# Kernel tuning notes

Hardware: AMD Instinct MI355X
Metric: run time of the kernel (lower is better)

## Reference

```python
import jax, jax.numpy as jnp
import numpy as np

N, E = 50000, 800000
IN_DIM, H, OUT_DIM = 128, 32, 128


def _p(key, shape, fan_in):
    return jax.random.normal(key, shape, dtype=jnp.float32) / np.float32(np.sqrt(fan_in))


def gcn(x, edge_index, W, b):
    # GCNConv with DOUBLED self-loops (outer add_self_loops + gcn_norm's own):
    # deg[i] = in_degree(i) + 2, each node receives 2*dinv[i]^2 * h[i].
    src, dst = edge_index[0], edge_index[1]
    h = x @ W  # [N, out]
    deg = jnp.zeros((x.shape[0],), h.dtype).at[dst].add(1.0) + 2.0
    dinv = jax.lax.rsqrt(deg)
    coef = dinv[src] * dinv[dst]  # [E]
    agg = jax.ops.segment_sum(h[src] * coef[:, None], dst, num_segments=x.shape[0])
    agg = agg + (2.0 * dinv * dinv)[:, None] * h
    return agg + b


def multihop(x, edge_index, W, b, fW, fb):
    # hop loop in the source always re-uses initial_x -> collapses to 1 pass
    return gcn(x, edge_index, W, b) @ fW + fb


def deconv(xc, W, b):
    # ConvTranspose1d(kernel=2, stride=2): out[n,o,2l+t] = sum_c xc[n,c,l]*W[c,o,t] + b[o]
    y = jnp.einsum('ncl,cot->nolt', xc, W) + b[None, :, None, None]
    return y.reshape(y.shape[0], y.shape[1], -1)  # [N, O, 2L]


def setup_inputs() -> dict:
    key = jax.random.key(0)
    ks = jax.random.split(key, 30)
    return {
        'x': jax.random.normal(ks[0], (N, IN_DIM), jnp.float32),
        'edge_index': jax.random.randint(ks[1], (2, E), 0, N),
        'w_enc1': _p(ks[2], (IN_DIM, H), IN_DIM), 'b_enc1': _p(ks[3], (H,), H),
        'fw_enc1': _p(ks[4], (H, H), H), 'fb_enc1': _p(ks[5], (H,), H),
        'w_enc2': _p(ks[6], (H, 2 * H), H), 'b_enc2': _p(ks[7], (2 * H,), 2 * H),
        'fw_enc2': _p(ks[8], (2 * H, 2 * H), 2 * H), 'fb_enc2': _p(ks[9], (2 * H,), 2 * H),
        'w_enc3': _p(ks[10], (2 * H, 4 * H), 2 * H), 'b_enc3': _p(ks[11], (4 * H,), 4 * H),
        'fw_enc3': _p(ks[12], (4 * H, 4 * H), 4 * H), 'fb_enc3': _p(ks[13], (4 * H,), 4 * H),
        'wd1': _p(ks[14], (4 * H, 2 * H, 2), 4 * H), 'bd1': _p(ks[15], (2 * H,), 4 * H),
        'wd2': _p(ks[16], (2 * H, H, 2), 2 * H), 'bd2': _p(ks[17], (H,), 2 * H),
        'wd3': _p(ks[18], (H, H, 2), H), 'bd3': _p(ks[19], (H,), H),
        'ws1': _p(ks[20], (2 * H, 2 * H), 2 * H), 'bs1': _p(ks[21], (2 * H,), 2 * H),
        'ws2': _p(ks[22], (H, H), H), 'bs2': _p(ks[23], (H,), H),
        'wf': _p(ks[24], (8 * H, OUT_DIM), 8 * H), 'bf': _p(ks[25], (OUT_DIM,), 8 * H),
    }


def reference(x, edge_index, w_enc1, b_enc1, fw_enc1, fb_enc1,
              w_enc2, b_enc2, fw_enc2, fb_enc2,
              w_enc3, b_enc3, fw_enc3, fb_enc3,
              wd1, bd1, wd2, bd2, wd3, bd3,
              ws1, bs1, ws2, bs2, wf, bf):
    relu = jax.nn.relu
    x1 = relu(multihop(x, edge_index, w_enc1, b_enc1, fw_enc1, fb_enc1))   # [N, H]
    x2 = relu(multihop(x1, edge_index, w_enc2, b_enc2, fw_enc2, fb_enc2))  # [N, 2H]
    x3 = relu(multihop(x2, edge_index, w_enc3, b_enc3, fw_enc3, fb_enc3))  # [N, 4H]
    d = deconv(x3[:, :, None], wd1, bd1)            # [N, 2H, 2]
    s2 = x2 @ ws1 + bs1                              # skip_conv1 (k=1) == linear
    d = d + s2[:, :, None]                           # repeat over length
    d = deconv(d, wd2, bd2)                          # [N, H, 4]
    s1 = x1 @ ws2 + bs2
    d = d + s1[:, :, None]
    d = deconv(d, wd3, bd3)                          # [N, H, 8]
    out = d.reshape(d.shape[0], -1) @ wf + bf        # [N, OUT_DIM]
    return out
```

## Files before the change

kernel.cpp:

```cpp
#include <hip/hip_runtime.h>

#define NN 50000
#define NE 800000
#define NBLK 196

typedef _Float16 half8 __attribute__((ext_vector_type(8)));
typedef _Float16 half4 __attribute__((ext_vector_type(4)));
typedef float f32x4v __attribute__((ext_vector_type(4)));

__global__ void k_zero2(int* __restrict__ bcnt) {
  bcnt[threadIdx.x] = 0;
}

__launch_bounds__(256)
__global__ void k_bcount(const int* __restrict__ dstv, int* __restrict__ bcnt) {
  __shared__ int cnt[256];
  int t = threadIdx.x;
  int e0 = blockIdx.x * 4096;
  cnt[t] = 0;
  __syncthreads();
#pragma unroll
  for (int i = 0; i < 16; ++i) {
    int e = e0 + i * 256 + t;
    if (e < NE) atomicAdd(&cnt[dstv[e] >> 8], 1);
  }
  __syncthreads();
  if (cnt[t] > 0) atomicAdd(&bcnt[t], cnt[t]);
}

__global__ void k_bscan(const int* __restrict__ bcnt, int* __restrict__ boff,
                        int* __restrict__ bcur, int* __restrict__ row_start) {
  __shared__ int s[256];
  int t = threadIdx.x;
  int v0 = (t < NBLK) ? bcnt[t] : 0;
  s[t] = v0;
  __syncthreads();
  for (int off = 1; off < 256; off <<= 1) {
    int v = (t >= off) ? s[t - off] : 0;
    __syncthreads();
    s[t] += v;
    __syncthreads();
  }
  int e = s[t] - v0;
  if (t < NBLK) { boff[t] = e; bcur[t] = e; }
  if (t == 0) { boff[NBLK] = NE; row_start[NN] = NE; }
}

__launch_bounds__(256)
__global__ void k_part1(const int* __restrict__ srcv, const int* __restrict__ dstv,
                        int* __restrict__ bcur, unsigned int* __restrict__ epk2) {
  __shared__ int cnt[256];
  __shared__ int base[256];
  int t = threadIdx.x;
  int e0 = blockIdx.x * 4096;
  cnt[t] = 0;
  __syncthreads();
  unsigned int pk[16];
  int lo[16], bk[16];
  bool ok[16];
#pragma unroll
  for (int i = 0; i < 16; ++i) {
    int e = e0 + i * 256 + t;
    ok[i] = (e < NE);
    if (ok[i]) {
      int s = srcv[e], d = dstv[e];
      bk[i] = d >> 8;
      pk[i] = (unsigned int)s | ((unsigned int)(d & 255) << 16);
      lo[i] = atomicAdd(&cnt[bk[i]], 1);
    }
  }
  __syncthreads();
  int c = cnt[t];
  if (c > 0) base[t] = atomicAdd(&bcur[t], c);
  __syncthreads();
#pragma unroll
  for (int i = 0; i < 16; ++i)
    if (ok[i]) epk2[base[bk[i]] + lo[i]] = pk[i];
}

__launch_bounds__(256)
__global__ void k_part2c(const unsigned int* __restrict__ epk2, const int* __restrict__ boff,
                         int* __restrict__ row_start, float* __restrict__ dinv,
                         float* __restrict__ rdinv, unsigned short* __restrict__ esrc) {
  __shared__ int cnt[256];
  __shared__ int cur[256];
  __shared__ int ss[256];
  int t = threadIdx.x;
  int b = blockIdx.x;
  int rs0 = boff[b], rs1 = boff[b + 1];
  cnt[t] = 0;
  __syncthreads();
  for (int i = rs0 + t; i < rs1; i += 256) {
    unsigned int p = epk2[i];
    atomicAdd(&cnt[(p >> 16) & 255], 1);
  }
  __syncthreads();
  int d = cnt[t];
  ss[t] = d;
  __syncthreads();
  for (int off = 1; off < 256; off <<= 1) {
    int v = (t >= off) ? ss[t - off] : 0;
    __syncthreads();
    ss[t] += v;
    __syncthreads();
  }
  int rs = rs0 + ss[t] - d;
  int node = b * 256 + t;
  if (node < NN) {
    row_start[node] = rs;
    float df = (float)d + 2.0f;
    dinv[node] = rsqrtf(df);
    rdinv[node] = sqrtf(df);
  }
  cur[t] = rs;
  __syncthreads();
  for (int i = rs0 + t; i < rs1; i += 256) {
    unsigned int p = epk2[i];
    int dl = (p >> 16) & 255;
    int tgt = atomicAdd(&cur[dl], 1);
    esrc[tgt] = (unsigned short)(p & 0xFFFFu);
  }
}

__global__ void k_prep1(const float* __restrict__ wd3, const float* __restrict__ wf,
                        const float* __restrict__ w2, const float* __restrict__ fw2,
                        const float* __restrict__ w3, const float* __restrict__ fw3,
                        const float* __restrict__ b1, const float* __restrict__ fw1,
                        const float* __restrict__ fb1,
                        const float* __restrict__ b2, const float* __restrict__ fb2,
                        const float* __restrict__ b3, const float* __restrict__ fb3,
                        float* __restrict__ G,
                        float* __restrict__ Wc2, float* __restrict__ Wc3,
                        float* __restrict__ bc1, float* __restrict__ bc2,
                        float* __restrict__ bc3) {
  int id = blockIdx.x * 256 + threadIdx.x;
  if (id < 16384) {
    int k = id & 127, r = id >> 7;
    int c = r >> 2, l = r & 3;
    float s = 0.f;
    for (int o = 0; o < 32; ++o) {
      s = fmaf(wd3[c * 64 + o * 2 + 0], wf[(o * 8 + 2 * l + 0) * 128 + k], s);
      s = fmaf(wd3[c * 64 + o * 2 + 1], wf[(o * 8 + 2 * l + 1) * 128 + k], s);
    }
    G[r * 128 + k] = s;
    return;
  }
  int id2 = id - 16384;
  if (id2 < 2048) {
    int c = id2 >> 6, k = id2 & 63;
    float s = 0.f;
    for (int j = 0; j < 64; ++j) s = fmaf(w2[c * 64 + j], fw2[j * 64 + k], s);
    Wc2[id2] = s;
  } else if (id2 < 10240) {
    int idx = id2 - 2048;
    int c = idx >> 7, k = idx & 127;
    float s = 0.f;
    for (int j = 0; j < 128; ++j) s = fmaf(w3[c * 128 + j], fw3[j * 128 + k], s);
    Wc3[idx] = s;
  } else if (id2 < 10272) {
    int k = id2 - 10240;
    float s = fb1[k];
    for (int j = 0; j < 32; ++j) s = fmaf(b1[j], fw1[j * 32 + k], s);
    bc1[k] = s;
  } else if (id2 < 10336) {
    int k = id2 - 10272;
    float s = fb2[k];
    for (int j = 0; j < 64; ++j) s = fmaf(b2[j], fw2[j * 64 + k], s);
    bc2[k] = s;
  } else if (id2 < 10464) {
    int k = id2 - 10336;
    float s = fb3[k];
    for (int j = 0; j < 128; ++j) s = fmaf(b3[j], fw3[j * 128 + k], s);
    bc3[k] = s;
  }
}

__global__ void k_prep_HA1(const float* __restrict__ wd2, const float* __restrict__ G,
                           const float* __restrict__ ws2,
                           float* __restrict__ Hm, float* __restrict__ A1) {
  int id = blockIdx.x * 256 + threadIdx.x;
  if (id < 16384) {
    int k = id & 127, r = id >> 7;
    int c = r >> 1, l = r & 1;
    float s = 0.f;
    for (int o = 0; o < 32; ++o) {
      s = fmaf(wd2[c * 64 + o * 2 + 0], G[(o * 4 + 2 * l + 0) * 128 + k], s);
      s = fmaf(wd2[c * 64 + o * 2 + 1], G[(o * 4 + 2 * l + 1) * 128 + k], s);
    }
    Hm[r * 128 + k] = s;
  } else if (id < 16384 + 4096) {
    int idx = id - 16384;
    int k = idx & 127, c = idx >> 7;
    float s = 0.f;
    for (int o = 0; o < 32; ++o) {
      float g = G[(4 * o) * 128 + k] + G[(4 * o + 1) * 128 + k] +
                G[(4 * o + 2) * 128 + k] + G[(4 * o + 3) * 128 + k];
      s = fmaf(ws2[c * 32 + o], g, s);
    }
    A1[c * 128 + k] = s;
  }
}

__global__ void k_prep_A32c0(const float* __restrict__ wd1, const float* __restrict__ ws1,
                             const float* __restrict__ Hm, const float* __restrict__ G,
                             const float* __restrict__ wf,
                             const float* __restrict__ bd1, const float* __restrict__ bs1,
                             const float* __restrict__ bd2, const float* __restrict__ bs2,
                             const float* __restrict__ bd3, const float* __restrict__ bf,
                             float* __restrict__ A3, float* __restrict__ A2,
                             float* __restrict__ c0) {
  int id = blockIdx.x * 256 + threadIdx.x;
  if (id < 16384) {
    int k = id & 127, c = id >> 7;
    float s = 0.f;
    for (int j = 0; j < 128; ++j) s = fmaf(wd1[c * 128 + j], Hm[j * 128 + k], s);
    A3[c * 128 + k] = s;
  } else if (id < 16384 + 8192) {
    int idx = id - 16384;
    int k = idx & 127, c = idx >> 7;
    float s = 0.f;
    for (int o = 0; o < 64; ++o)
      s = fmaf(ws1[c * 64 + o], Hm[(2 * o) * 128 + k] + Hm[(2 * o + 1) * 128 + k], s);
    A2[c * 128 + k] = s;
  } else if (id < 16384 + 8192 + 128) {
    int k = id - 16384 - 8192;
    float s = bf[k];
    for (int o = 0; o < 64; ++o) {
      float b = bd1[o] + bs1[o];
      s = fmaf(b, Hm[(o * 2) * 128 + k] + Hm[(o * 2 + 1) * 128 + k], s);
    }
    for (int o = 0; o < 32; ++o) {
      float b = bd2[o] + bs2[o];
      float g = G[(o * 4) * 128 + k] + G[(o * 4 + 1) * 128 + k] +
                G[(o * 4 + 2) * 128 + k] + G[(o * 4 + 3) * 128 + k];
      s = fmaf(b, g, s);
    }
    for (int o = 0; o < 32; ++o) {
      float w8 = 0.f;
      for (int j = 0; j < 8; ++j) w8 += wf[(o * 8 + j) * 128 + k];
      s = fmaf(bd3[o], w8, s);
    }
    c0[k] = s;
  }
}

__global__ void k_prep_pack(const float* __restrict__ Wc3, const float* __restrict__ Acat,
                            _Float16* __restrict__ W3pk, _Float16* __restrict__ Apk) {
  int id = blockIdx.x * 256 + threadIdx.x;
  if (id < 1024) {
    int l = id & 63, nb = (id >> 6) & 7, kb = id >> 9;
    int kbase = kb * 32 + ((l >> 4) << 3);
    int col = nb * 16 + (l & 15);
#pragma unroll
    for (int j = 0; j < 8; ++j)
      W3pk[id * 8 + j] = (_Float16)Wc3[(kbase + j) * 128 + col];
  } else if (id < 1024 + 3584) {
    int idx = id - 1024;
    int l = idx & 63, nb = (idx >> 6) & 7, kb = idx >> 9;
    int kbase = kb * 32 + ((l >> 4) << 3);
    int col = nb * 16 + (l & 15);
#pragma unroll
    for (int j = 0; j < 8; ++j)
      Apk[idx * 8 + j] = (_Float16)Acat[(kbase + j) * 128 + col];
  }
}

__launch_bounds__(256)
__global__ void k_gemm1t(const float* __restrict__ X, const float* __restrict__ W,
                         const float* __restrict__ dinv, _Float16* __restrict__ Yh) {
  __shared__ float sW[128 * 32];
  __shared__ float sXc[128 * 33];
  int t = threadIdx.x;
  int n0 = blockIdx.x * 128;
#pragma unroll
  for (int it = 0; it < 4; ++it) {
    int idx = t + it * 256;
    int kr = idx >> 3, c4 = (idx & 7) * 4;
    *reinterpret_cast<float4*>(&sW[kr * 32 + c4]) =
        *reinterpret_cast<const float4*>(&W[kr * 32 + c4]);
  }
  int rg = t >> 3;
  int cg = t & 7;
  float acc[4][4];
#pragma unroll
  for (int r = 0; r < 4; ++r)
#pragma unroll
    for (int c = 0; c < 4; ++c) acc[r][c] = 0.f;

  for (int ch = 0; ch < 4; ++ch) {
    __syncthreads();
#pragma unroll
    for (int it = 0; it < 4; ++it) {
      int idx = t + it * 256;
      int row = idx & 127, k4 = (idx >> 7) * 4;
      int n = n0 + row;
      float4 v = make_float4(0.f, 0.f, 0.f, 0.f);
      if (n < NN) v = *reinterpret_cast<const float4*>(&X[(size_t)n * 128 + ch * 32 + k4]);
      sXc[row * 33 + k4 + 0] = v.x;
      sXc[row * 33 + k4 + 1] = v.y;
      sXc[row * 33 + k4 + 2] = v.z;
      sXc[row * 33 + k4 + 3] = v.w;
    }
    __syncthreads();
#pragma unroll
    for (int k = 0; k < 32; ++k) {
      float4 w = *reinterpret_cast<const float4*>(&sW[(ch * 32 + k) * 32 + cg * 4]);
#pragma unroll
      for (int r = 0; r < 4; ++r) {
        float xv = sXc[(rg * 4 + r) * 33 + k];
        acc[r][0] = fmaf(xv, w.x, acc[r][0]);
        acc[r][1] = fmaf(xv, w.y, acc[r][1]);
        acc[r][2] = fmaf(xv, w.z, acc[r][2]);
        acc[r][3] = fmaf(xv, w.w, acc[r][3]);
      }
    }
  }
#pragma unroll
  for (int r = 0; r < 4; ++r) {
    int n = n0 + rg * 4 + r;
    if (n < NN) {
      float dv = dinv[n];
      half4 hv;
      hv[0] = (_Float16)(dv * acc[r][0]); hv[1] = (_Float16)(dv * acc[r][1]);
      hv[2] = (_Float16)(dv * acc[r][2]); hv[3] = (_Float16)(dv * acc[r][3]);
      *reinterpret_cast<half4*>(&Yh[(size_t)n * 32 + cg * 4]) = hv;
    }
  }
}

__device__ inline float4 gsum32h(const half4* __restrict__ H4,
                                 const unsigned short* __restrict__ esrc,
                                 const int* __restrict__ row_start,
                                 int n, int fg, int way) {
  float4 acc = make_float4(0.f, 0.f, 0.f, 0.f);
  if (way == 0) {
    half4 h = H4[(size_t)n * 8 + fg];
    acc.x = 2.f * (float)h[0]; acc.y = 2.f * (float)h[1];
    acc.z = 2.f * (float)h[2]; acc.w = 2.f * (float)h[3];
  }
  int end = row_start[n + 1];
  int i = row_start[n] + way;
  for (; i + 4 < end; i += 8) {
    int s0 = esrc[i], s1 = esrc[i + 4];
    half4 a = H4[(size_t)s0 * 8 + fg];
    half4 b = H4[(size_t)s1 * 8 + fg];
    acc.x += (float)a[0] + (float)b[0];
    acc.y += (float)a[1] + (float)b[1];
    acc.z += (float)a[2] + (float)b[2];
    acc.w += (float)a[3] + (float)b[3];
  }
  if (i < end) {
    int s = esrc[i];
    half4 a = H4[(size_t)s * 8 + fg];
    acc.x += (float)a[0]; acc.y += (float)a[1];
    acc.z += (float)a[2]; acc.w += (float)a[3];
  }
  acc.x += __shfl_xor(acc.x, 8);  acc.y += __shfl_xor(acc.y, 8);
  acc.z += __shfl_xor(acc.z, 8);  acc.w += __shfl_xor(acc.w, 8);
  acc.x += __shfl_xor(acc.x, 16); acc.y += __shfl_xor(acc.y, 16);
  acc.z += __shfl_xor(acc.z, 16); acc.w += __shfl_xor(acc.w, 16);
  return acc;
}

__launch_bounds__(256)
__global__ void k_fuse1(const _Float16* __restrict__ H, const unsigned short* __restrict__ esrc,
                        const int* __restrict__ row_start, const float* __restrict__ dinv,
                        const float* __restrict__ W, const float* __restrict__ bias,
                        _Float16* __restrict__ Y) {
  __shared__ float sZT[32][9];
  __shared__ float sW[32 * 32];
  int t = threadIdx.x;
  int n0 = blockIdx.x * 8;
  {
    int kr = t >> 3, c4 = (t & 7) * 4;
    *reinterpret_cast<float4*>(&sW[kr * 32 + c4]) =
        *reinterpret_cast<const float4*>(&W[kr * 32 + c4]);
  }
  int node = t >> 5, fg = t & 7, way = (t >> 3) & 3;
  int n = n0 + node;
  float4 z = gsum32h(reinterpret_cast<const half4*>(H), esrc, row_start, n, fg, way);
  if (way == 0) {
    float dv = dinv[n];
    sZT[fg * 4 + 0][node] = dv * z.x;
    sZT[fg * 4 + 1][node] = dv * z.y;
    sZT[fg * 4 + 2][node] = dv * z.z;
    sZT[fg * 4 + 3][node] = dv * z.w;
  }
  __syncthreads();
  int nd = t >> 5, col = t & 31;
  float a = bias[col];
#pragma unroll
  for (int k = 0; k < 32; ++k) a = fmaf(sZT[k][nd], sW[k * 32 + col], a);
  Y[(size_t)(n0 + nd) * 32 + col] = (_Float16)(dinv[n0 + nd] * fmaxf(a, 0.f));
}

__launch_bounds__(256)
__global__ void k_fuse2(const _Float16* __restrict__ H, const unsigned short* __restrict__ esrc,
                        const int* __restrict__ row_start, const float* __restrict__ dinv,
                        const float* __restrict__ W, const float* __restrict__ bias,
                        _Float16* __restrict__ Y) {
  __shared__ float sZT[32][9];
  __shared__ float sW[32 * 64];
  int t = threadIdx.x;
  int n0 = blockIdx.x * 8;
#pragma unroll
  for (int it = 0; it < 2; ++it) {
    int idx = t + it * 256;
    int kr = idx >> 4, c4 = (idx & 15) * 4;
    *reinterpret_cast<float4*>(&sW[kr * 64 + c4]) =
        *reinterpret_cast<const float4*>(&W[kr * 64 + c4]);
  }
  int node = t >> 5, fg = t & 7, way = (t >> 3) & 3;
  int n = n0 + node;
  float4 z = gsum32h(reinterpret_cast<const half4*>(H), esrc, row_start, n, fg, way);
  if (way == 0) {
    float dv = dinv[n];
    sZT[fg * 4 + 0][node] = dv * z.x;
    sZT[fg * 4 + 1][node] = dv * z.y;
    sZT[fg * 4 + 2][node] = dv * z.z;
    sZT[fg * 4 + 3][node] = dv * z.w;
  }
  __syncthreads();
  int nd = t >> 5, col = t & 31;
  float a = bias[col], b = bias[col + 32];
#pragma unroll
  for (int k = 0; k < 32; ++k) {
    float zv = sZT[k][nd];
    a = fmaf(zv, sW[k * 64 + col], a);
    b = fmaf(zv, sW[k * 64 + col + 32], b);
  }
  float dv = dinv[n0 + nd];
  Y[(size_t)(n0 + nd) * 64 + col] = (_Float16)(dv * fmaxf(a, 0.f));
  Y[(size_t)(n0 + nd) * 64 + col + 32] = (_Float16)(dv * fmaxf(b, 0.f));
}

__launch_bounds__(256)
__global__ void k_gath64(const _Float16* __restrict__ H, const unsigned short* __restrict__ esrc,
                         const int* __restrict__ row_start, const float* __restrict__ dinv,
                         _Float16* __restrict__ Zh) {
  int t = threadIdx.x;
  int n = blockIdx.x * 4 + (t >> 6);
  int fg = t & 15, way = (t >> 4) & 3;
  const half4* H4 = reinterpret_cast<const half4*>(H);
  float4 acc = make_float4(0.f, 0.f, 0.f, 0.f);
  if (way == 0) {
    half4 h = H4[(size_t)n * 16 + fg];
    acc.x = 2.f * (float)h[0]; acc.y = 2.f * (float)h[1];
    acc.z = 2.f * (float)h[2]; acc.w = 2.f * (float)h[3];
  }
  int end = row_start[n + 1];
  int i = row_start[n] + way;
  for (; i + 4 < end; i += 8) {
    int s0 = esrc[i], s1 = esrc[i + 4];
    half4 a = H4[(size_t)s0 * 16 + fg];
    half4 b = H4[(size_t)s1 * 16 + fg];
    acc.x += (float)a[0] + (float)b[0];
    acc.y += (float)a[1] + (float)b[1];
    acc.z += (float)a[2] + (float)b[2];
    acc.w += (float)a[3] + (float)b[3];
  }
  if (i < end) {
    int s = esrc[i];
    half4 a = H4[(size_t)s * 16 + fg];
    acc.x += (float)a[0]; acc.y += (float)a[1];
    acc.z += (float)a[2]; acc.w += (float)a[3];
  }
  acc.x += __shfl_xor(acc.x, 16); acc.y += __shfl_xor(acc.y, 16);
  acc.z += __shfl_xor(acc.z, 16); acc.w += __shfl_xor(acc.w, 16);
  acc.x += __shfl_xor(acc.x, 32); acc.y += __shfl_xor(acc.y, 32);
  acc.z += __shfl_xor(acc.z, 32); acc.w += __shfl_xor(acc.w, 32);
  if (way == 0) {
    float dv = dinv[n];
    half4 hv;
    hv[0] = (_Float16)(dv * acc.x); hv[1] = (_Float16)(dv * acc.y);
    hv[2] = (_Float16)(dv * acc.z); hv[3] = (_Float16)(dv * acc.w);
    *reinterpret_cast<half4*>(Zh + (size_t)n * 64 + fg * 4) = hv;
  }
}

__device__ inline half8 cvt8h(const _Float16* __restrict__ p, float s) {
  half8 v = *reinterpret_cast<const half8*>(p);
  half8 a;
#pragma unroll
  for (int i = 0; i < 8; ++i) a[i] = (_Float16)(s * (float)v[i]);
  return a;
}

__launch_bounds__(256)
__global__ void k_decode(const _Float16* __restrict__ z3h, const _Float16* __restrict__ X2h,
                         const _Float16* __restrict__ X1h, const float* __restrict__ rdinv,
                         const half8* __restrict__ W3pk, const half8* __restrict__ Apk,
                         const float* __restrict__ bc3, const float* __restrict__ c0,
                         float* __restrict__ out) {
  __shared__ _Float16 sX3[4][16][136];
  int t = threadIdx.x;
  int w = t >> 6, l = t & 63;
  int m16 = l & 15, g = l >> 4;
  int n0 = blockIdx.x * 64 + w * 16;
  int nrow = n0 + m16;

  f32x4v acc[8];
#pragma unroll
  for (int nb = 0; nb < 8; ++nb) {
    float bv = bc3[nb * 16 + m16];
    acc[nb] = (f32x4v){bv, bv, bv, bv};
  }
#pragma unroll
  for (int kb = 0; kb < 2; ++kb) {
    half8 a = *reinterpret_cast<const half8*>(z3h + (size_t)nrow * 64 + kb * 32 + g * 8);
#pragma unroll
    for (int nb = 0; nb < 8; ++nb) {
      half8 b = W3pk[(kb * 8 + nb) * 64 + l];
      acc[nb] = __builtin_amdgcn_mfma_f32_16x16x32_f16(a, b, acc[nb], 0, 0, 0);
    }
  }
#pragma unroll
  for (int nb = 0; nb < 8; ++nb)
#pragma unroll
    for (int r = 0; r < 4; ++r)
      sX3[w][g * 4 + r][nb * 16 + m16] = (_Float16)fmaxf(acc[nb][r], 0.0f);
  __syncthreads();

  float rd = rdinv[nrow];
#pragma unroll
  for (int nb = 0; nb < 8; ++nb) {
    float cv = c0[nb * 16 + m16];
    acc[nb] = (f32x4v){cv, cv, cv, cv};
  }
#pragma unroll
  for (int kb = 0; kb < 7; ++kb) {
    half8 a;
    if (kb < 4)
      a = *reinterpret_cast<const half8*>(&sX3[w][m16][kb * 32 + g * 8]);
    else if (kb < 6)
      a = cvt8h(X2h + (size_t)nrow * 64 + (kb - 4) * 32 + g * 8, rd);
    else
      a = cvt8h(X1h + (size_t)nrow * 32 + g * 8, rd);
#pragma unroll
    for (int nb = 0; nb < 8; ++nb) {
      half8 b = Apk[(kb * 8 + nb) * 64 + l];
      acc[nb] = __builtin_amdgcn_mfma_f32_16x16x32_f16(a, b, acc[nb], 0, 0, 0);
    }
  }
#pragma unroll
  for (int nb = 0; nb < 8; ++nb)
#pragma unroll
    for (int r = 0; r < 4; ++r) {
      int n = n0 + g * 4 + r;
      if (n < NN) out[(size_t)n * 128 + nb * 16 + m16] = acc[nb][r];
    }
}

extern "C" void kernel_launch(void* const* d_in, const int* in_sizes, int n_in,
                              void* d_out, int out_size, void* d_ws, size_t ws_size,
                              hipStream_t stream) {
  const float* x   = (const float*)d_in[0];
  const int* ei    = (const int*)d_in[1];
  const int* srcv  = ei;
  const int* dstv  = ei + NE;
  const float* w1  = (const float*)d_in[2];
  const float* b1  = (const float*)d_in[3];
  const float* fw1 = (const float*)d_in[4];
  const float* fb1 = (const float*)d_in[5];
  const float* w2  = (const float*)d_in[6];
  const float* b2  = (const float*)d_in[7];
  const float* fw2 = (const float*)d_in[8];
  const float* fb2 = (const float*)d_in[9];
  const float* w3  = (const float*)d_in[10];
  const float* b3  = (const float*)d_in[11];
  const float* fw3 = (const float*)d_in[12];
  const float* fb3 = (const float*)d_in[13];
  const float* wd1 = (const float*)d_in[14];
  const float* bd1 = (const float*)d_in[15];
  const float* wd2 = (const float*)d_in[16];
  const float* bd2 = (const float*)d_in[17];
  const float* wd3 = (const float*)d_in[18];
  const float* bd3 = (const float*)d_in[19];
  const float* ws1 = (const float*)d_in[20];
  const float* bs1 = (const float*)d_in[21];
  const float* ws2 = (const float*)d_in[22];
  const float* bs2 = (const float*)d_in[23];
  const float* wf  = (const float*)d_in[24];
  const float* bf  = (const float*)d_in[25];

  float* fp = (float*)d_ws;
  float* dinv = fp;
  float* rdinv= dinv + 50176;
  _Float16* h1h = (_Float16*)(rdinv + 50176);
  _Float16* x1h = h1h + 1601536;
  _Float16* x2h = x1h + 1601536;
  _Float16* z3h = x2h + 3203072;
  float* Wc2  = (float*)(z3h + 3203072);
  float* Wc3  = Wc2 + 2048;
  float* bc1  = Wc3 + 8192;
  float* bc2  = bc1 + 64;
  float* bc3  = bc2 + 64;
  float* G    = bc3 + 128;
  float* Hm   = G + 16384;
  float* A3   = Hm + 16384;
  float* A2   = A3 + 16384;
  float* A1   = A2 + 8192;
  float* c0   = A1 + 4096;
  _Float16* W3pk = (_Float16*)(c0 + 256);
  _Float16* Apk  = W3pk + 8192;
  unsigned int* epk2 = (unsigned int*)(Apk + 28672);
  unsigned short* esrc = (unsigned short*)(epk2 + 800000);
  int* ip     = (int*)(esrc + 800128);
  int* row_start = ip;
  int* bcnt   = row_start + 50176;
  int* boff   = bcnt + 256;
  int* bcur   = boff + 260;

  float* outp = (float*)d_out;

  k_zero2<<<1, 256, 0, stream>>>(bcnt);
  k_bcount<<<(NE + 4095) / 4096, 256, 0, stream>>>(dstv, bcnt);
  k_bscan<<<1, 256, 0, stream>>>(bcnt, boff, bcur, row_start);
  k_part1<<<(NE + 4095) / 4096, 256, 0, stream>>>(srcv, dstv, bcur, epk2);
  k_part2c<<<NBLK, 256, 0, stream>>>(epk2, boff, row_start, dinv, rdinv, esrc);

  k_prep1<<<105, 256, 0, stream>>>(wd3, wf, w2, fw2, w3, fw3, b1, fw1, fb1,
                                   b2, fb2, b3, fb3, G, Wc2, Wc3, bc1, bc2, bc3);
  k_prep_HA1<<<80, 256, 0, stream>>>(wd2, G, ws2, Hm, A1);
  k_prep_A32c0<<<97, 256, 0, stream>>>(wd1, ws1, Hm, G, wf, bd1, bs1, bd2, bs2, bd3, bf,
                                       A3, A2, c0);
  k_prep_pack<<<18, 256, 0, stream>>>(Wc3, A3 , W3pk, Apk);

  k_gemm1t<<<(NN + 127) / 128, 256, 0, stream>>>(x, w1, dinv, h1h);
  k_fuse1<<<NN / 8, 256, 0, stream>>>(h1h, esrc, row_start, dinv, fw1, bc1, x1h);
  k_fuse2<<<NN / 8, 256, 0, stream>>>(x1h, esrc, row_start, dinv, Wc2, bc2, x2h);
  k_gath64<<<NN / 4, 256, 0, stream>>>(x2h, esrc, row_start, dinv, z3h);
  k_decode<<<(NN + 63) / 64, 256, 0, stream>>>(z3h, x2h, x1h, rdinv, (const half8*)W3pk,
                                               (const half8*)Apk, bc3, c0, outp);
}
```

Before: 171.2 us.

## Merge preprocessing kernels into four launches and move first GEMM to MFMA

Combines the CSR-construction stages with the weight-folding prep kernels into four multi-role launches, with block-index ranges choosing each role. This removes the zeroing and separate count launches by writing per-block bucket counts that the scan block then sums. The first dense projection now packs w1 to fp16 and computes on 16x16x32 fp16 MFMA instead of the fp32 shared-memory FMA kernel. This cuts launch count and serialization, at the cost of fp16 rounding of x and w1 and a serial 196-way reduction in the scan block.

```diff
diff --git a/kernel.cpp b/kernel.cpp
--- a/kernel.cpp
+++ b/kernel.cpp
@@ -8,177 +8,119 @@
 typedef _Float16 half4 __attribute__((ext_vector_type(4)));
 typedef float f32x4v __attribute__((ext_vector_type(4)));
 
-__global__ void k_zero2(int* __restrict__ bcnt) {
-  bcnt[threadIdx.x] = 0;
-}
-
-__launch_bounds__(256)
-__global__ void k_bcount(const int* __restrict__ dstv, int* __restrict__ bcnt) {
+__launch_bounds__(256)
+__global__ void k_u1(const int* __restrict__ dstv, int* __restrict__ bcnt2,
+                     const float* __restrict__ wd3, const float* __restrict__ wf,
+                     const float* __restrict__ w2, const float* __restrict__ fw2,
+                     const float* __restrict__ w3, const float* __restrict__ fw3,
+                     const float* __restrict__ b1, const float* __restrict__ fw1,
+                     const float* __restrict__ fb1,
+                     const float* __restrict__ b2, const float* __restrict__ fb2,
+                     const float* __restrict__ b3, const float* __restrict__ fb3,
+                     float* __restrict__ G,
+                     float* __restrict__ Wc2, float* __restrict__ Wc3,
+                     float* __restrict__ bc1, float* __restrict__ bc2,
+                     float* __restrict__ bc3,
+                     const float* __restrict__ w1, _Float16* __restrict__ W1pk) {
   __shared__ int cnt[256];
   int t = threadIdx.x;
-  int e0 = blockIdx.x * 4096;
-  cnt[t] = 0;
-  __syncthreads();
-#pragma unroll
-  for (int i = 0; i < 16; ++i) {
-    int e = e0 + i * 256 + t;
-    if (e < NE) atomicAdd(&cnt[dstv[e] >> 8], 1);
-  }
-  __syncthreads();
-  if (cnt[t] > 0) atomicAdd(&bcnt[t], cnt[t]);
-}
-
-__global__ void k_bscan(const int* __restrict__ bcnt, int* __restrict__ boff,
-                        int* __restrict__ bcur, int* __restrict__ row_start) {
-  __shared__ int s[256];
-  int t = threadIdx.x;
-  int v0 = (t < NBLK) ? bcnt[t] : 0;
-  s[t] = v0;
-  __syncthreads();
-  for (int off = 1; off < 256; off <<= 1) {
-    int v = (t >= off) ? s[t - off] : 0;
-    __syncthreads();
-    s[t] += v;
-    __syncthreads();
-  }
-  int e = s[t] - v0;
-  if (t < NBLK) { boff[t] = e; bcur[t] = e; }
-  if (t == 0) { boff[NBLK] = NE; row_start[NN] = NE; }
-}
-
-__launch_bounds__(256)
-__global__ void k_part1(const int* __restrict__ srcv, const int* __restrict__ dstv,
-                        int* __restrict__ bcur, unsigned int* __restrict__ epk2) {
-  __shared__ int cnt[256];
-  __shared__ int base[256];
-  int t = threadIdx.x;
-  int e0 = blockIdx.x * 4096;
-  cnt[t] = 0;
-  __syncthreads();
-  unsigned int pk[16];
-  int lo[16], bk[16];
-  bool ok[16];
-#pragma unroll
-  for (int i = 0; i < 16; ++i) {
-    int e = e0 + i * 256 + t;
-    ok[i] = (e < NE);
-    if (ok[i]) {
-      int s = srcv[e], d = dstv[e];
-      bk[i] = d >> 8;
-      pk[i] = (unsigned int)s | ((unsigned int)(d & 255) << 16);
-      lo[i] = atomicAdd(&cnt[bk[i]], 1);
-    }
-  }
-  __syncthreads();
-  int c = cnt[t];
-  if (c > 0) base[t] = atomicAdd(&bcur[t], c);
-  __syncthreads();
-#pragma unroll
-  for (int i = 0; i < 16; ++i)
-    if (ok[i]) epk2[base[bk[i]] + lo[i]] = pk[i];
-}
-
-__launch_bounds__(256)
-__global__ void k_part2c(const unsigned int* __restrict__ epk2, const int* __restrict__ boff,
-                         int* __restrict__ row_start, float* __restrict__ dinv,
-                         float* __restrict__ rdinv, unsigned short* __restrict__ esrc) {
-  __shared__ int cnt[256];
-  __shared__ int cur[256];
-  __shared__ int ss[256];
-  int t = threadIdx.x;
   int b = blockIdx.x;
-  int rs0 = boff[b], rs1 = boff[b + 1];
-  cnt[t] = 0;
-  __syncthreads();
-  for (int i = rs0 + t; i < rs1; i += 256) {
-    unsigned int p = epk2[i];
-    atomicAdd(&cnt[(p >> 16) & 255], 1);
-  }
-  __syncthreads();
-  int d = cnt[t];
-  ss[t] = d;
-  __syncthreads();
-  for (int off = 1; off < 256; off <<= 1) {
-    int v = (t >= off) ? ss[t - off] : 0;
-    __syncthreads();
-    ss[t] += v;
-    __syncthreads();
-  }
-  int rs = rs0 + ss[t] - d;
-  int node = b * 256 + t;
-  if (node < NN) {
-    row_start[node] = rs;
-    float df = (float)d + 2.0f;
-    dinv[node] = rsqrtf(df);
-    rdinv[node] = sqrtf(df);
-  }
-  cur[t] = rs;
-  __syncthreads();
-  for (int i = rs0 + t; i < rs1; i += 256) {
-    unsigned int p = epk2[i];
-    int dl = (p >> 16) & 255;
-    int tgt = atomicAdd(&cur[dl], 1);
-    esrc[tgt] = (unsigned short)(p & 0xFFFFu);
-  }
-}
-
-__global__ void k_prep1(const float* __restrict__ wd3, const float* __restrict__ wf,
-                        const float* __restrict__ w2, const float* __restrict__ fw2,
-                        const float* __restrict__ w3, const float* __restrict__ fw3,
-                        const float* __restrict__ b1, const float* __restrict__ fw1,
-                        const float* __restrict__ fb1,
-                        const float* __restrict__ b2, const float* __restrict__ fb2,
-                        const float* __restrict__ b3, const float* __restrict__ fb3,
-                        float* __restrict__ G,
-                        float* __restrict__ Wc2, float* __restrict__ Wc3,
-                        float* __restrict__ bc1, float* __restrict__ bc2,
-                        float* __restrict__ bc3) {
-  int id = blockIdx.x * 256 + threadIdx.x;
-  if (id < 16384) {
-    int k = id & 127, r = id >> 7;
-    int c = r >> 2, l = r & 3;
-    float s = 0.f;
-    for (int o = 0; o < 32; ++o) {
-      s = fmaf(wd3[c * 64 + o * 2 + 0], wf[(o * 8 + 2 * l + 0) * 128 + k], s);
-      s = fmaf(wd3[c * 64 + o * 2 + 1], wf[(o * 8 + 2 * l + 1) * 128 + k], s);
-    }
-    G[r * 128 + k] = s;
+  if (b < NBLK) {
+    int e0 = b * 4096;
+    cnt[t] = 0;
+    __syncthreads();
+#pragma unroll
+    for (int i = 0; i < 16; ++i) {
+      int e = e0 + i * 256 + t;
+      if (e < NE) atomicAdd(&cnt[dstv[e] >> 8], 1);
+    }
+    __syncthreads();
+    bcnt2[b * 256 + t] = cnt[t];
     return;
   }
-  int id2 = id - 16384;
-  if (id2 < 2048) {
-    int c = id2 >> 6, k = id2 & 63;
-    float s = 0.f;
-    for (int j = 0; j < 64; ++j) s = fmaf(w2[c * 64 + j], fw2[j * 64 + k], s);
-    Wc2[id2] = s;
-  } else if (id2 < 10240) {
-    int idx = id2 - 2048;
-    int c = idx >> 7, k = idx & 127;
-    float s = 0.f;
-    for (int j = 0; j < 128; ++j) s = fmaf(w3[c * 128 + j], fw3[j * 128 + k], s);
-    Wc3[idx] = s;
-  } else if (id2 < 10272) {
-    int k = id2 - 10240;
-    float s = fb1[k];
-    for (int j = 0; j < 32; ++j) s = fmaf(b1[j], fw1[j * 32 + k], s);
-    bc1[k] = s;
-  } else if (id2 < 10336) {
-    int k = id2 - 10272;
-    float s = fb2[k];
-    for (int j = 0; j < 64; ++j) s = fmaf(b2[j], fw2[j * 64 + k], s);
-    bc2[k] = s;
-  } else if (id2 < 10464) {
-    int k = id2 - 10336;
-    float s = fb3[k];
-    for (int j = 0; j < 128; ++j) s = fmaf(b3[j], fw3[j * 128 + k], s);
-    bc3[k] = s;
-  }
-}
-
-__global__ void k_prep_HA1(const float* __restrict__ wd2, const float* __restrict__ G,
-                           const float* __restrict__ ws2,
-                           float* __restrict__ Hm, float* __restrict__ A1) {
-  int id = blockIdx.x * 256 + threadIdx.x;
+  if (b < NBLK + 105) {
+    int id = (b - NBLK) * 256 + t;
+    if (id < 16384) {
+      int k = id & 127, r = id >> 7;
+      int c = r >> 2, l = r & 3;
+      float s = 0.f;
+      for (int o = 0; o < 32; ++o) {
+        s = fmaf(wd3[c * 64 + o * 2 + 0], wf[(o * 8 + 2 * l + 0) * 128 + k], s);
+        s = fmaf(wd3[c * 64 + o * 2 + 1], wf[(o * 8 + 2 * l + 1) * 128 + k], s);
+      }
+      G[r * 128 + k] = s;
+      return;
+    }
+    int id2 = id - 16384;
+    if (id2 < 2048) {
+      int c = id2 >> 6, k = id2 & 63;
+      float s = 0.f;
+      for (int j = 0; j < 64; ++j) s = fmaf(w2[c * 64 + j], fw2[j * 64 + k], s);
+      Wc2[id2] = s;
+    } else if (id2 < 10240) {
+      int idx = id2 - 2048;
+      int c = idx >> 7, k = idx & 127;
+      float s = 0.f;
+      for (int j = 0; j < 128; ++j) s = fmaf(w3[c * 128 + j], fw3[j * 128 + k], s);
+      Wc3[idx] = s;
+    } else if (id2 < 10272) {
+      int k = id2 - 10240;
+      float s = fb1[k];
+      for (int j = 0; j < 32; ++j) s = fmaf(b1[j], fw1[j * 32 + k], s);
+      bc1[k] = s;
+    } else if (id2 < 10336) {
+      int k = id2 - 10272;
+      float s = fb2[k];
+      for (int j = 0; j < 64; ++j) s = fmaf(b2[j], fw2[j * 64 + k], s);
+      bc2[k] = s;
+    } else if (id2 < 10464) {
+      int k = id2 - 10336;
+      float s = fb3[k];
+      for (int j = 0; j < 128; ++j) s = fmaf(b3[j], fw3[j * 128 + k], s);
+      bc3[k] = s;
+    }
+    return;
+  }
+#pragma unroll
+  for (int it = 0; it < 2; ++it) {
+    int id = t + it * 256;
+    int l = id & 63, f = id >> 6;
+    int kb = f >> 1, nb = f & 1;
+    int kbase = kb * 32 + ((l >> 4) << 3);
+    int col = nb * 16 + (l & 15);
+#pragma unroll
+    for (int j = 0; j < 8; ++j)
+      W1pk[id * 8 + j] = (_Float16)w1[(kbase + j) * 32 + col];
+  }
+}
+
+__launch_bounds__(256)
+__global__ void k_u2(const int* __restrict__ bcnt2, int* __restrict__ boff,
+                     int* __restrict__ bcur, int* __restrict__ row_start,
+                     const float* __restrict__ wd2, const float* __restrict__ G,
+                     const float* __restrict__ ws2,
+                     float* __restrict__ Hm, float* __restrict__ A1) {
+  int t = threadIdx.x;
+  int b = blockIdx.x;
+  if (b == 0) {
+    __shared__ int s[256];
+    int v0 = 0;
+    if (t < NBLK)
+      for (int blk = 0; blk < NBLK; ++blk) v0 += bcnt2[blk * 256 + t];
+    s[t] = v0;
+    __syncthreads();
+    for (int off = 1; off < 256; off <<= 1) {
+      int v = (t >= off) ? s[t - off] : 0;
+      __syncthreads();
+      s[t] += v;
+      __syncthreads();
+    }
+    int e = s[t] - v0;
+    if (t < NBLK) { boff[t] = e; bcur[t] = e; }
+    if (t == 0) { boff[NBLK] = NE; row_start[NN] = NE; }
+    return;
+  }
+  int id = (b - 1) * 256 + t;
   if (id < 16384) {
     int k = id & 127, r = id >> 7;
     int c = r >> 1, l = r & 1;
@@ -201,15 +143,49 @@
   }
 }
 
-__global__ void k_prep_A32c0(const float* __restrict__ wd1, const float* __restrict__ ws1,
-                             const float* __restrict__ Hm, const float* __restrict__ G,
-                             const float* __restrict__ wf,
-                             const float* __restrict__ bd1, const float* __restrict__ bs1,
-                             const float* __restrict__ bd2, const float* __restrict__ bs2,
-                             const float* __restrict__ bd3, const float* __restrict__ bf,
-                             float* __restrict__ A3, float* __restrict__ A2,
-                             float* __restrict__ c0) {
-  int id = blockIdx.x * 256 + threadIdx.x;
+__launch_bounds__(256)
+__global__ void k_u3(const int* __restrict__ srcv, const int* __restrict__ dstv,
+                     int* __restrict__ bcur, unsigned int* __restrict__ epk2,
+                     const float* __restrict__ wd1, const float* __restrict__ ws1,
+                     const float* __restrict__ Hm, const float* __restrict__ G,
+                     const float* __restrict__ wf,
+                     const float* __restrict__ bd1, const float* __restrict__ bs1,
+                     const float* __restrict__ bd2, const float* __restrict__ bs2,
+                     const float* __restrict__ bd3, const float* __restrict__ bf,
+                     float* __restrict__ A3, float* __restrict__ A2,
+                     float* __restrict__ c0) {
+  __shared__ int cnt[256];
+  __shared__ int base[256];
+  int t = threadIdx.x;
+  int b = blockIdx.x;
+  if (b < NBLK) {
+    int e0 = b * 4096;
+    cnt[t] = 0;
+    __syncthreads();
+    unsigned int pk[16];
+    int lo[16], bk[16];
+    bool ok[16];
+#pragma unroll
+    for (int i = 0; i < 16; ++i) {
+      int e = e0 + i * 256 + t;
+      ok[i] = (e < NE);
+      if (ok[i]) {
+        int s = srcv[e], d = dstv[e];
+        bk[i] = d >> 8;
+        pk[i] = (unsigned int)s | ((unsigned int)(d & 255) << 16);
+        lo[i] = atomicAdd(&cnt[bk[i]], 1);
+      }
+    }
+    __syncthreads();
+    int c = cnt[t];
+    if (c > 0) base[t] = atomicAdd(&bcur[t], c);
+    __syncthreads();
+#pragma unroll
+    for (int i = 0; i < 16; ++i)
+      if (ok[i]) epk2[base[bk[i]] + lo[i]] = pk[i];
+    return;
+  }
+  int id = (b - NBLK) * 256 + t;
   if (id < 16384) {
     int k = id & 127, c = id >> 7;
     float s = 0.f;
@@ -226,14 +202,14 @@
     int k = id - 16384 - 8192;
     float s = bf[k];
     for (int o = 0; o < 64; ++o) {
-      float b = bd1[o] + bs1[o];
-      s = fmaf(b, Hm[(o * 2) * 128 + k] + Hm[(o * 2 + 1) * 128 + k], s);
+      float bb = bd1[o] + bs1[o];
+      s = fmaf(bb, Hm[(o * 2) * 128 + k] + Hm[(o * 2 + 1) * 128 + k], s);
     }
     for (int o = 0; o < 32; ++o) {
-      float b = bd2[o] + bs2[o];
+      float bb = bd2[o] + bs2[o];
       float g = G[(o * 4) * 128 + k] + G[(o * 4 + 1) * 128 + k] +
                 G[(o * 4 + 2) * 128 + k] + G[(o * 4 + 3) * 128 + k];
-      s = fmaf(b, g, s);
+      s = fmaf(bb, g, s);
     }
     for (int o = 0; o < 32; ++o) {
       float w8 = 0.f;
@@ -244,9 +220,54 @@
   }
 }
 
-__global__ void k_prep_pack(const float* __restrict__ Wc3, const float* __restrict__ Acat,
-                            _Float16* __restrict__ W3pk, _Float16* __restrict__ Apk) {
-  int id = blockIdx.x * 256 + threadIdx.x;
+__launch_bounds__(256)
+__global__ void k_u4(const unsigned int* __restrict__ epk2, const int* __restrict__ boff,
+                     int* __restrict__ row_start, float* __restrict__ dinv,
+                     float* __restrict__ rdinv, unsigned short* __restrict__ esrc,
+                     const float* __restrict__ Wc3, const float* __restrict__ Acat,
+                     _Float16* __restrict__ W3pk, _Float16* __restrict__ Apk) {
+  int t = threadIdx.x;
+  int b = blockIdx.x;
+  if (b < NBLK) {
+    __shared__ int cnt[256];
+    __shared__ int cur[256];
+    __shared__ int ss[256];
+    int rs0 = boff[b], rs1 = boff[b + 1];
+    cnt[t] = 0;
+    __syncthreads();
+    for (int i = rs0 + t; i < rs1; i += 256) {
+      unsigned int p = epk2[i];
+      atomicAdd(&cnt[(p >> 16) & 255], 1);
+    }
+    __syncthreads();
+    int d = cnt[t];
+    ss[t] = d;
+    __syncthreads();
+    for (int off = 1; off < 256; off <<= 1) {
+      int v = (t >= off) ? ss[t - off] : 0;
+      __syncthreads();
+      ss[t] += v;
+      __syncthreads();
+    }
+    int rs = rs0 + ss[t] - d;
+    int node = b * 256 + t;
+    if (node < NN) {
+      row_start[node] = rs;
+      float df = (float)d + 2.0f;
+      dinv[node] = rsqrtf(df);
+      rdinv[node] = sqrtf(df);
+    }
+    cur[t] = rs;
+    __syncthreads();
+    for (int i = rs0 + t; i < rs1; i += 256) {
+      unsigned int p = epk2[i];
+      int dl = (p >> 16) & 255;
+      int tgt = atomicAdd(&cur[dl], 1);
+      esrc[tgt] = (unsigned short)(p & 0xFFFFu);
+    }
+    return;
+  }
+  int id = (b - NBLK) * 256 + t;
   if (id < 1024) {
     int l = id & 63, nb = (id >> 6) & 7, kb = id >> 9;
     int kbase = kb * 32 + ((l >> 4) << 3);
@@ -265,67 +286,43 @@
   }
 }
 
-__launch_bounds__(256)
-__global__ void k_gemm1t(const float* __restrict__ X, const float* __restrict__ W,
+__device__ inline half8 cvt8f(const float* __restrict__ p) {
+  float4 u = *reinterpret_cast<const float4*>(p);
+  float4 v = *reinterpret_cast<const float4*>(p + 4);
+  half8 a;
+  a[0] = (_Float16)u.x; a[1] = (_Float16)u.y; a[2] = (_Float16)u.z; a[3] = (_Float16)u.w;
+  a[4] = (_Float16)v.x; a[5] = (_Float16)v.y; a[6] = (_Float16)v.z; a[7] = (_Float16)v.w;
+  return a;
+}
+
+__launch_bounds__(256)
+__global__ void k_gemm1m(const float* __restrict__ X, const half8* __restrict__ W1pk,
                          const float* __restrict__ dinv, _Float16* __restrict__ Yh) {
-  __shared__ float sW[128 * 32];
-  __shared__ float sXc[128 * 33];
-  int t = threadIdx.x;
-  int n0 = blockIdx.x * 128;
-#pragma unroll
-  for (int it = 0; it < 4; ++it) {
-    int idx = t + it * 256;
-    int kr = idx >> 3, c4 = (idx & 7) * 4;
-    *reinterpret_cast<float4*>(&sW[kr * 32 + c4]) =
-        *reinterpret_cast<const float4*>(&W[kr * 32 + c4]);
-  }
-  int rg = t >> 3;
-  int cg = t & 7;
-  float acc[4][4];
-#pragma unroll
-  for (int r = 0; r < 4; ++r)
-#pragma unroll
-    for (int c = 0; c < 4; ++c) acc[r][c] = 0.f;
-
-  for (int ch = 0; ch < 4; ++ch) {
-    __syncthreads();
-#pragma unroll
-    for (int it = 0; it < 4; ++it) {
-      int idx = t + it * 256;
-      int row = idx & 127, k4 = (idx >> 7) * 4;
-      int n = n0 + row;
-      float4 v = make_float4(0.f, 0.f, 0.f, 0.f);
-      if (n < NN) v = *reinterpret_cast<const float4*>(&X[(size_t)n * 128 + ch * 32 + k4]);
-      sXc[row * 33 + k4 + 0] = v.x;
-      sXc[row * 33 + k4 + 1] = v.y;
-      sXc[row * 33 + k4 + 2] = v.z;
-      sXc[row * 33 + k4 + 3] = v.w;
-    }
-    __syncthreads();
-#pragma unroll
-    for (int k = 0; k < 32; ++k) {
-      float4 w = *reinterpret_cast<const float4*>(&sW[(ch * 32 + k) * 32 + cg * 4]);
-#pragma unroll
-      for (int r = 0; r < 4; ++r) {
-        float xv = sXc[(rg * 4 + r) * 33 + k];
-        acc[r][0] = fmaf(xv, w.x, acc[r][0]);
-        acc[r][1] = fmaf(xv, w.y, acc[r][1]);
-        acc[r][2] = fmaf(xv, w.z, acc[r][2]);
-        acc[r][3] = fmaf(xv, w.w, acc[r][3]);
-      }
-    }
-  }
-#pragma unroll
-  for (int r = 0; r < 4; ++r) {
-    int n = n0 + rg * 4 + r;
-    if (n < NN) {
-      float dv = dinv[n];
-      half4 hv;
-      hv[0] = (_Float16)(dv * acc[r][0]); hv[1] = (_Float16)(dv * acc[r][1]);
-      hv[2] = (_Float16)(dv * acc[r][2]); hv[3] = (_Float16)(dv * acc[r][3]);
-      *reinterpret_cast<half4*>(&Yh[(size_t)n * 32 + cg * 4]) = hv;
-    }
-  }
+  int t = threadIdx.x;
+  int w = t >> 6, l = t & 63;
+  int m16 = l & 15, g = l >> 4;
+  int n0 = blockIdx.x * 64 + w * 16;
+  int nrow = n0 + m16;
+  f32x4v acc[2];
+  acc[0] = (f32x4v){0.f, 0.f, 0.f, 0.f};
+  acc[1] = (f32x4v){0.f, 0.f, 0.f, 0.f};
+#pragma unroll
+  for (int kb = 0; kb < 4; ++kb) {
+    half8 a = (half8)(_Float16)0.f;
+    if (nrow < NN) a = cvt8f(X + (size_t)nrow * 128 + kb * 32 + g * 8);
+#pragma unroll
+    for (int nb = 0; nb < 2; ++nb)
+      acc[nb] = __builtin_amdgcn_mfma_f32_16x16x32_f16(a, W1pk[(kb * 2 + nb) * 64 + l],
+                                                       acc[nb], 0, 0, 0);
+  }
+#pragma unroll
+  for (int nb = 0; nb < 2; ++nb)
+#pragma unroll
+    for (int r = 0; r < 4; ++r) {
+      int n = n0 + g * 4 + r;
+      if (n < NN)
+        Yh[(size_t)n * 32 + nb * 16 + m16] = (_Float16)(dinv[n] * acc[nb][r]);
+    }
 }
 
 __device__ inline float4 gsum32h(const half4* __restrict__ H4,
@@ -603,30 +600,29 @@
   float* c0   = A1 + 4096;
   _Float16* W3pk = (_Float16*)(c0 + 256);
   _Float16* Apk  = W3pk + 8192;
-  unsigned int* epk2 = (unsigned int*)(Apk + 28672);
+  _Float16* W1pk = Apk + 28672;
+  unsigned int* epk2 = (unsigned int*)(W1pk + 4096);
   unsigned short* esrc = (unsigned short*)(epk2 + 800000);
   int* ip     = (int*)(esrc + 800128);
   int* row_start = ip;
-  int* bcnt   = row_start + 50176;
-  int* boff   = bcnt + 256;
+  int* bcnt2  = row_start + 50176;
+  int* boff   = bcnt2 + 50176;
   int* bcur   = boff + 260;
 
   float* outp = (float*)d_out;
 
-  k_zero2<<<1, 256, 0, stream>>>(bcnt);
-  k_bcount<<<(NE + 4095) / 4096, 256, 0, stream>>>(dstv, bcnt);
-  k_bscan<<<1, 256, 0, stream>>>(bcnt, boff, bcur, row_start);
-  k_part1<<<(NE + 4095) / 4096, 256, 0, stream>>>(srcv, dstv, bcur, epk2);
-  k_part2c<<<NBLK, 256, 0, stream>>>(epk2, boff, row_start, dinv, rdinv, esrc);
-
-  k_prep1<<<105, 256, 0, stream>>>(wd3, wf, w2, fw2, w3, fw3, b1, fw1, fb1,
-                                   b2, fb2, b3, fb3, G, Wc2, Wc3, bc1, bc2, bc3);
-  k_prep_HA1<<<80, 256, 0, stream>>>(wd2, G, ws2, Hm, A1);
-  k_prep_A32c0<<<97, 256, 0, stream>>>(wd1, ws1, Hm, G, wf, bd1, bs1, bd2, bs2, bd3, bf,
-                                       A3, A2, c0);
-  k_prep_pack<<<18, 256, 0, stream>>>(Wc3, A3 , W3pk, Apk);
-
-  k_gemm1t<<<(NN + 127) / 128, 256, 0, stream>>>(x, w1, dinv, h1h);
+  k_u1<<<NBLK + 105 + 1, 256, 0, stream>>>(dstv, bcnt2,
+                                           wd3, wf, w2, fw2, w3, fw3, b1, fw1, fb1,
+                                           b2, fb2, b3, fb3, G, Wc2, Wc3, bc1, bc2, bc3,
+                                           w1, W1pk);
+  k_u2<<<1 + 80, 256, 0, stream>>>(bcnt2, boff, bcur, row_start, wd2, G, ws2, Hm, A1);
+  k_u3<<<NBLK + 97, 256, 0, stream>>>(srcv, dstv, bcur, epk2,
+                                      wd1, ws1, Hm, G, wf, bd1, bs1, bd2, bs2, bd3, bf,
+                                      A3, A2, c0);
+  k_u4<<<NBLK + 18, 256, 0, stream>>>(epk2, boff, row_start, dinv, rdinv, esrc,
+                                      Wc3, A3 , W3pk, Apk);
+
+  k_gemm1m<<<(NN + 63) / 64, 256, 0, stream>>>(x, (const half8*)W1pk, dinv, h1h);
   k_fuse1<<<NN / 8, 256, 0, stream>>>(h1h, esrc, row_start, dinv, fw1, bc1, x1h);
   k_fuse2<<<NN / 8, 256, 0, stream>>>(x1h, esrc, row_start, dinv, Wc2, bc2, x2h);
   k_gath64<<<NN / 4, 256, 0, stream>>>(x2h, esrc, row_start, dinv, z3h);
```

Result: faster. 147.2 us (-14.1%).
